# Optimization experiments

Hardware: AMD Instinct MI355X
Metric: run time of the kernel (lower is better)

The kernel has to match this reference:

```python
import jax, jax.numpy as jnp
import numpy as np

PAD = 0
NEG = -1e9
POSV = 1e9

def ln(x, eps=1e-5):
    m = jnp.mean(x, -1, keepdims=True)
    v = jnp.mean((x - m) ** 2, -1, keepdims=True)
    return (x - m) * jax.lax.rsqrt(v + eps)

def conv1d(h, w, b, shift):
    # h: [B,L,H], w: [K,H,H] (WIO). Even kernel -> pad K//2 both sides then drop first output (torch layers.Conv1d shift).
    K = w.shape[0]
    p = K // 2 if shift else (K - 1) // 2
    out = jax.lax.conv_general_dilated(h, w, (1,), [(p, p)], dimension_numbers=('NWC', 'WIO', 'NWC')) + b
    return out[:, 1:, :] if shift else out

def _forward(x, pos, emb, parser_conv_w, parser_conv_b, dist_conv_w, dist_conv_b, dist_lin_w, dist_lin_b, height_w1, height_b1, height_w2, height_b2, rel_weight_raw, scaler_raw, attn_ln_g, attn_ln_b, qw, qb, kw, kb, vw, vb, ow, ob, ff_ln_g, ff_ln_b, ff_w1, ff_b1, ff_w2, ff_b2, final_ln_g, final_ln_b, out_bias):
    B, L = x.shape
    NL, NH, _ = rel_weight_raw.shape
    H = emb.shape[1]
    mask = x != PAD
    mask_shift = jnp.concatenate([mask[:, 1:], jnp.zeros((B, 1), bool)], 1)

    # ---- parser: conv + LN(no affine) + tanh stack ----
    h = emb[x]
    for i in range(parser_conv_w.shape[0]):
        h = jnp.where(mask[:, :, None], h, 0.0)
        h = jnp.tanh(ln(conv1d(h, parser_conv_w[i], parser_conv_b[i], False)))
    height = (jnp.tanh(ln(h @ height_w1 + height_b1)) @ height_w2 + height_b2)[..., 0]
    height = jnp.where(mask, height, NEG)
    distance = (jnp.tanh(ln(conv1d(h, dist_conv_w, dist_conv_b, True))) @ dist_lin_w + dist_lin_b)[..., 0]
    distance = jnp.where(mask_shift, distance, POSV)

    # ---- margin normalization of distance vs running height max ----
    hm = jnp.triu(jnp.broadcast_to(height[:, None, :], (B, L, L))) - jnp.tril(jnp.full((B, L, L), POSV, jnp.float32), -1)
    hm = jnp.triu(jax.lax.cummax(hm, axis=2))
    d_pad = jnp.concatenate([jnp.full((B, 1), POSV, jnp.float32), distance[:, :-1]], 1)
    margin = jnp.triu(jnp.minimum(jax.nn.relu(d_pad[:, :, None] - hm), jax.nn.relu(distance[:, None, :] - hm)))
    mm = jnp.concatenate([mask_shift[:, None, :], jnp.broadcast_to(mask[:, None, :], (B, L - 1, L))], 1)
    distance = distance - jnp.max(jnp.where(mm, margin, 0.0))

    # ---- block decomposition via cummin (flip+cummin) and cumsum ----
    scaler = jnp.exp(scaler_raw)
    gamma = jax.nn.sigmoid(-(distance[:, None, :] - height[:, :, None]) * scaler[0])
    ones = jnp.ones_like(gamma)
    bml = jax.lax.cummin(jnp.tril(gamma, -1) + jnp.triu(ones), axis=2, reverse=True)
    bml = jnp.tril(bml - jnp.concatenate([jnp.zeros((B, L, 1)), bml[:, :, :-1]], 2))
    xr = jnp.triu(gamma) + jnp.tril(ones, -1)
    bmr = jax.lax.cummin(jnp.concatenate([jnp.ones((B, L, 1)), xr[:, :, :-1]], 2), axis=2)
    bmr = jnp.triu(bmr - jnp.concatenate([bmr[:, :, 1:], jnp.zeros((B, L, 1))], 2))
    block_p = bml[:, :, :, None] * bmr[:, :, None, :]  # [B,L,L,L]
    block = jnp.tril(jnp.cumsum(bml, 2)) + jnp.triu(jnp.cumsum(bmr[:, :, ::-1], 2)[:, :, ::-1], 1)

    # ---- head distribution: softmax of height over span i<=k<=j ----
    idx = jnp.arange(L)
    hmask = (idx[:, None, None] <= idx[None, None, :]) & (idx[None, None, :] <= idx[None, :, None])
    head_p = jax.nn.softmax(jnp.where(hmask[None], (height * scaler[1])[:, None, None, :], NEG), axis=-1)  # [B,L,L,L]
    head = jnp.einsum('blij,bijh->blh', block_p, head_p)
    eye = jnp.eye(L, dtype=bool)[None]
    head = jnp.where(eye, 0.0, head)
    child = jnp.swapaxes(head, 1, 2)
    cibling = jnp.where(eye, 0.0, head @ child)
    rel = jnp.stack([head, child], 1)  # relations = ('head','child')
    rel_w = jax.nn.softmax(rel_weight_raw, -1)  # weight_act = 'softmax'
    dep = jnp.einsum('lhr,brij->lbhij', rel_w, rel)  # [NL,B,NH,L,L]

    # ---- transformer: sigmoid(QK^T) * structural mask (eval mode, no dropout) ----
    kpm = jnp.where(mask, 0.0, NEG)[:, None, None, :]
    hd = H // NH
    h = emb[x]
    for i in range(NL):
        z = ln(h) * attn_ln_g[i] + attn_ln_b[i]
        q = ((z @ qw[i] + qb[i]) * (hd ** -0.5)).reshape(B, L, NH, hd)
        k = (z @ kw[i] + kb[i]).reshape(B, L, NH, hd)
        v = (z @ vw[i] + vb[i]).reshape(B, L, NH, hd)
        w = jax.nn.sigmoid(jnp.einsum('blhd,bmhd->bhlm', q, k) + kpm) * dep[i]
        o = jnp.einsum('bhlm,bmhd->blhd', w, v).reshape(B, L, H)
        h = h + (o @ ow[i] + ob[i])
        f = ln(h) * ff_ln_g[i] + ff_ln_b[i]
        h = h + (jax.nn.leaky_relu(f @ ff_w1[i] + ff_b1[i]) @ ff_w2[i] + ff_b2[i])
    raw = ln(h) * final_ln_g + final_ln_b
    return (raw @ emb.T + out_bias).reshape(B * L, -1)  # tied output embedding

def setup_inputs():
    key = jax.random.key(0)
    ks = iter(jax.random.split(key, 64))
    B, L, H, V = 8, 128, 512, 10000
    NL, NH, FF = 8, 8, 2048
    def rn(shape, sc=0.02):
        return jax.random.normal(next(ks), shape, jnp.float32) * sc
    return dict(
        x=jax.random.randint(next(ks), (B, L), 0, V),
        pos=jnp.tile(jnp.arange(L)[None, :], (B, 1)),
        emb=rn((V, H), 0.05),
        parser_conv_w=rn((4, 9, H, H)), parser_conv_b=rn((4, H)),
        dist_conv_w=rn((2, H, H)), dist_conv_b=rn((H,)),
        dist_lin_w=rn((H, 1)), dist_lin_b=rn((1,)),
        height_w1=rn((H, H)), height_b1=rn((H,)),
        height_w2=rn((H, 1)), height_b2=rn((1,)),
        rel_weight_raw=rn((NL, NH, 2), 0.1),
        scaler_raw=rn((2,), 0.1),
        attn_ln_g=jnp.ones((NL, H)), attn_ln_b=jnp.zeros((NL, H)),
        qw=rn((NL, H, H)), qb=rn((NL, H)),
        kw=rn((NL, H, H)), kb=rn((NL, H)),
        vw=rn((NL, H, H)), vb=rn((NL, H)),
        ow=rn((NL, H, H)), ob=rn((NL, H)),
        ff_ln_g=jnp.ones((NL, H)), ff_ln_b=jnp.zeros((NL, H)),
        ff_w1=rn((NL, H, FF)), ff_b1=rn((NL, FF)),
        ff_w2=rn((NL, FF, H)), ff_b2=rn((NL, H)),
        final_ln_g=jnp.ones((H,)), final_ln_b=jnp.zeros((H,)),
        out_bias=jnp.zeros((V,)),
    )

def reference(x, pos, emb, parser_conv_w, parser_conv_b, dist_conv_w, dist_conv_b, dist_lin_w, dist_lin_b, height_w1, height_b1, height_w2, height_b2, rel_weight_raw, scaler_raw, attn_ln_g, attn_ln_b, qw, qb, kw, kb, vw, vb, ow, ob, ff_ln_g, ff_ln_b, ff_w1, ff_b1, ff_w2, ff_b2, final_ln_g, final_ln_b, out_bias):
    return _forward(x, pos, emb, parser_conv_w, parser_conv_b, dist_conv_w, dist_conv_b, dist_lin_w, dist_lin_b, height_w1, height_b1, height_w2, height_b2, rel_weight_raw, scaler_raw, attn_ln_g, attn_ln_b, qw, qb, kw, kb, vw, vb, ow, ob, ff_ln_g, ff_ln_b, ff_w1, ff_b1, ff_w2, ff_b2, final_ln_g, final_ln_b, out_bias)
```

## Files before the change

### kernel.cpp

```cpp
#include <hip/hip_runtime.h>
#include <hip/hip_bf16.h>

typedef __hip_bfloat16 bf16;
typedef __attribute__((ext_vector_type(8))) short short8;
typedef __attribute__((ext_vector_type(4))) float f32x4;

static __device__ __forceinline__ float b2f(bf16 x){ return __bfloat162float(x); }
static __device__ __forceinline__ bf16  f2b(float x){ return __float2bfloat16(x); }
static __device__ __forceinline__ short f2bs(float x){ bf16 h = f2b(x); short s; __builtin_memcpy(&s, &h, 2); return s; }

#define GLOBAL_AS __attribute__((address_space(1)))
#define LDS_AS    __attribute__((address_space(3)))
static __device__ __forceinline__ void gll16(const void* g, short* l){
  __builtin_amdgcn_global_load_lds((const GLOBAL_AS void*)g, (LDS_AS void*)l, 16, 0, 0);
}


constexpr size_t AL2(size_t x){ return (x + 255) & ~(size_t)255; }
constexpr size_t SCAL_OFF  = 0;
constexpr size_t BIASF_OFF = AL2(SCAL_OFF + 256*4);
constexpr size_t MASK_OFF  = AL2(BIASF_OFF + 50176*4);
constexpr size_t HEIGHT_OFF= AL2(MASK_OFF + 1024*4);
constexpr size_t DIST_OFF  = AL2(HEIGHT_OFF + 1024*4);
constexpr size_t E_OFF     = AL2(DIST_OFF + 1024*4);
constexpr size_t P_OFF     = AL2(E_OFF + 1024*4);
constexpr size_t H0_OFF    = AL2(P_OFF + 8*132*4);
constexpr size_t TMPF_OFF  = AL2(H0_OFF + (size_t)1024*512*4);
constexpr size_t HMBF_OFF  = AL2(TMPF_OFF + (size_t)1024*512*4);
constexpr size_t HBF_OFF   = AL2(HMBF_OFF + (size_t)1024*512*2);
constexpr size_t ZBF_OFF   = AL2(HBF_OFF + (size_t)1024*512*2);
constexpr size_t QKV_OFF   = AL2(ZBF_OFF + (size_t)1024*512*2);
constexpr size_t VT_OFF    = AL2(QKV_OFF + (size_t)1024*1536*2);
constexpr size_t WATT_OFF  = AL2(VT_OFF + (size_t)64*64*128*2);
constexpr size_t OBF_OFF   = AL2(WATT_OFF + (size_t)64*128*128*2);
constexpr size_t FF1_OFF   = AL2(OBF_OFF + (size_t)1024*512*2);
constexpr size_t ACOL_OFF  = AL2(FF1_OFF + (size_t)1024*2048*2);
constexpr size_t BML_OFF   = AL2(ACOL_OFF + (size_t)1024*4608*2);
constexpr size_t BMR_OFF   = AL2(BML_OFF + (size_t)8*128*128*4);
constexpr size_t HEADP_OFF = AL2(BMR_OFF + (size_t)8*128*128*4);
constexpr size_t PWT_OFF   = AL2(HEADP_OFF + (size_t)8*128*128*4);
constexpr size_t DWT_OFF   = AL2(PWT_OFF + (size_t)4*4608*512*2);
constexpr size_t HW1T_OFF  = AL2(DWT_OFF + (size_t)1024*512*2);
constexpr size_t QKVT_OFF  = AL2(HW1T_OFF + (size_t)512*512*2);
constexpr size_t OWT_OFF   = AL2(QKVT_OFF + (size_t)8*1536*512*2);
constexpr size_t F1T_OFF   = AL2(OWT_OFF + (size_t)8*512*512*2);
constexpr size_t F2T_OFF   = AL2(F1T_OFF + (size_t)8*2048*512*2);
constexpr size_t WS_NEED   = AL2(F2T_OFF + (size_t)8*512*2048*2);

__global__ __launch_bounds__(256) void prep_k(
    const float* pcb, const float* dcb, const float* hb1,
    const float* qb, const float* kb, const float* vb, const float* ob,
    const float* fb1, const float* fb2, const float* outb,
    const float* relraw, const float* sraw,
    float* biasf, float* scal)
{
  int i = blockIdx.x*256 + threadIdx.x;
  if      (i < 2048)  biasf[i] = pcb[i];
  else if (i < 2560)  biasf[i] = dcb[i-2048];
  else if (i < 3072)  biasf[i] = hb1[i-2560];
  else if (i < 15360){ int j = i-3072; int l = j/1536, n = j%1536;
    biasf[i] = (n<512 ? qb[l*512+n] : n<1024 ? kb[l*512+n-512] : vb[l*512+n-1024]); }
  else if (i < 19456) biasf[i] = ob[i-15360];
  else if (i < 35840) biasf[i] = fb1[i-19456];
  else if (i < 39936) biasf[i] = fb2[i-35840];
  else if (i < 49936) biasf[i] = outb[i-39936];
  else if (i == 49936) scal[0] = expf(sraw[0]);
  else if (i == 49937) scal[1] = expf(sraw[1]);
  else if (i == 49938) scal[2] = 0.f;
  else if (i < 49939 + 128){ int q = i - 49939; int p = q>>1;
    float e0 = expf(relraw[2*p]), e1 = expf(relraw[2*p+1]);
    float r0 = e0/(e0+e1);
    scal[4 + q] = (q&1) ? (1.f - r0) : r0; }
}

struct TP {
  const float *pw, *dw, *hw1, *qw, *kw, *vw, *ow, *f1, *f2;
  bf16 *pwT, *dwT, *hw1T, *qkvT, *owT, *f1T, *f2T;
};
__global__ __launch_bounds__(256) void transpose_all_k(TP tp){
  __shared__ short tl[32*33];
  int blk = blockIdx.x, t = threadIdx.x;
  const float* src; bf16* dst; int R, C, tile;
  if      (blk < 9216){ int l = blk/2304; tile = blk%2304; src = tp.pw + (size_t)l*2359296; dst = tp.pwT + (size_t)l*2359296; R=4608; C=512; }
  else if (blk < 9728){ tile = blk-9216; src = tp.dw;  dst = tp.dwT;  R=1024; C=512; }
  else if (blk < 9984){ tile = blk-9728; src = tp.hw1; dst = tp.hw1T; R=512;  C=512; }
  else if (blk < 12032){ int j=blk-9984;  int l=j>>8; tile=j&255;  src = tp.qw + (size_t)l*262144; dst = tp.qkvT + (size_t)l*786432;           R=512; C=512; }
  else if (blk < 14080){ int j=blk-12032; int l=j>>8; tile=j&255;  src = tp.kw + (size_t)l*262144; dst = tp.qkvT + (size_t)l*786432 + 262144;  R=512; C=512; }
  else if (blk < 16128){ int j=blk-14080; int l=j>>8; tile=j&255;  src = tp.vw + (size_t)l*262144; dst = tp.qkvT + (size_t)l*786432 + 524288;  R=512; C=512; }
  else if (blk < 18176){ int j=blk-16128; int l=j>>8; tile=j&255;  src = tp.ow + (size_t)l*262144; dst = tp.owT + (size_t)l*262144;            R=512; C=512; }
  else if (blk < 26368){ int j=blk-18176; int l=j>>10; tile=j&1023; src = tp.f1 + (size_t)l*1048576; dst = tp.f1T + (size_t)l*1048576;         R=512; C=2048; }
  else                 { int j=blk-26368; int l=j>>10; tile=j&1023; src = tp.f2 + (size_t)l*1048576; dst = tp.f2T + (size_t)l*1048576;         R=2048; C=512; }
  int tc = C >> 5;
  int r0 = (tile/tc)*32, c0 = (tile%tc)*32;
  int tx = t & 31, ty = t >> 5;
  short* d = (short*)dst;
  #pragma unroll
  for (int p=0;p<4;p++){ int r = ty + p*8; tl[r*33+tx] = f2bs(src[(size_t)(r0+r)*C + c0 + tx]); }
  __syncthreads();
  #pragma unroll
  for (int p=0;p<4;p++){ int cc = ty + p*8; d[(size_t)(c0+cc)*R + r0 + tx] = tl[tx*33+cc]; }
}

__global__ __launch_bounds__(256) void embed_k(const int* x, const float* emb, float* h0, bf16* hm, int* mask){
  int m = blockIdx.x, t = threadIdx.x;
  int xi = x[m]; int mk = (xi != 0) ? 1 : 0;
  if (t == 0) mask[m] = mk;
  const float* e = emb + (size_t)xi*512;
  float e0 = e[t], e1 = e[t+256];
  h0[(size_t)m*512+t]     = e0;
  h0[(size_t)m*512+t+256] = e1;
  bf16 z = f2b(0.f);
  hm[(size_t)m*512+t]     = mk ? f2b(e0) : z;
  hm[(size_t)m*512+t+256] = mk ? f2b(e1) : z;
}

__global__ __launch_bounds__(256) void embcast_k(const float* e, bf16* o){
  size_t i = (size_t)blockIdx.x*1024 + threadIdx.x*4;
  float4 v = *(const float4*)(e + i);
  o[i]   = f2b(v.x); o[i+1] = f2b(v.y);
  o[i+2] = f2b(v.z); o[i+3] = f2b(v.w);
}

__global__ __launch_bounds__(64) void im2col9_k(const bf16* hsrc, bf16* acol){
  int m = blockIdx.x, k = blockIdx.y, t = threadIdx.x;
  int tt = m & 127; int st = tt + k - 4;
  int4* dst = (int4*)(acol + (size_t)m*4608 + (size_t)k*512);
  if (st >= 0 && st < 128){ const int4* s = (const int4*)(hsrc + (size_t)(m + k - 4)*512); dst[t] = s[t]; }
  else dst[t] = make_int4(0,0,0,0);
}
__global__ __launch_bounds__(64) void im2col2_k(const bf16* hsrc, bf16* acol){
  int m = blockIdx.x, k = blockIdx.y, t = threadIdx.x;
  int tt = m & 127; int st = tt + k;
  int4* dst = (int4*)(acol + (size_t)m*1024 + (size_t)k*512);
  if (st < 128){ const int4* s = (const int4*)(hsrc + (size_t)(m + k)*512); dst[t] = s[t]; }
  else dst[t] = make_int4(0,0,0,0);
}

__device__ __forceinline__ float blkSum256(float v, float* red){
  #pragma unroll
  for (int o=32;o>0;o>>=1) v += __shfl_down(v, o);
  __syncthreads();
  if ((threadIdx.x & 63) == 0) red[threadIdx.x >> 6] = v;
  __syncthreads();
  return red[0]+red[1]+red[2]+red[3];
}
__global__ __launch_bounds__(256) void ln_tanh_k(const float* X, const float* bias, bf16* outm, bf16* outp, const int* mask){
  __shared__ float red[4];
  int row = blockIdx.x, t = threadIdx.x;
  const float* x = X + (size_t)row*512;
  float a0 = x[t] + bias[t], a1 = x[t+256] + bias[t+256];
  float mean = blkSum256(a0+a1, red)*(1.f/512.f);
  float d0 = a0-mean, d1 = a1-mean;
  float var = blkSum256(d0*d0+d1*d1, red)*(1.f/512.f);
  float inv = rsqrtf(var + 1e-5f);
  float y0 = tanhf(d0*inv), y1 = tanhf(d1*inv);
  int mk = mask[row];
  size_t o = (size_t)row*512 + t;
  outp[o] = f2b(y0); outp[o+256] = f2b(y1);
  outm[o] = mk ? f2b(y0) : f2b(0.f);
  outm[o+256] = mk ? f2b(y1) : f2b(0.f);
}
__global__ __launch_bounds__(256) void ln_affine_k(const float* X, const float* g, const float* bb, bf16* out){
  __shared__ float red[4];
  int row = blockIdx.x, t = threadIdx.x;
  const float* x = X + (size_t)row*512;
  float a0 = x[t], a1 = x[t+256];
  float mean = blkSum256(a0+a1, red)*(1.f/512.f);
  float d0 = a0-mean, d1 = a1-mean;
  float var = blkSum256(d0*d0+d1*d1, red)*(1.f/512.f);
  float inv = rsqrtf(var + 1e-5f);
  size_t o = (size_t)row*512 + t;
  out[o]     = f2b(d0*inv*g[t]     + bb[t]);
  out[o+256] = f2b(d1*inv*g[t+256] + bb[t+256]);
}

__global__ __launch_bounds__(256) void rowdot_k(const bf16* X, const float* w, const float* bsc,
                                                const int* mask, float* out, int mode){
  int wv = threadIdx.x>>6, lane = threadIdx.x&63;
  int m = blockIdx.x*4 + wv;
  const bf16* x = X + (size_t)m*512;
  float s = 0.f;
  #pragma unroll
  for (int i=0;i<8;++i){ int c = i*64 + lane; s += b2f(x[c])*w[c]; }
  #pragma unroll
  for (int o=32;o>0;o>>=1) s += __shfl_down(s,o);
  if (lane==0){
    float v = s + bsc[0];
    if (mode==0) out[m] = (mask[m]!=0) ? v : -1e9f;
    else { int tt = m & 127; bool ms = (tt<127) && (mask[m+1]!=0); out[m] = ms ? v : 1e9f; }
  }
}

__global__ __launch_bounds__(128) void margin_k(const float* height, const float* dist, const int* mask, float* scal){
  int b = blockIdx.x, i = threadIdx.x;
  __shared__ float hg[128], ds[128], red[128];
  hg[i] = height[b*128+i]; ds[i] = dist[b*128+i];
  __syncthreads();
  float dpi = (i==0) ? 1e9f : ds[i-1];
  float hmr = -3.0e38f, best = 0.f;
  for (int j=i; j<128; ++j){
    hmr = fmaxf(hmr, hg[j]);
    float mg = fminf(fmaxf(dpi - hmr, 0.f), fmaxf(ds[j] - hmr, 0.f));
    bool mm = (i==0) ? ((j<127) && (mask[b*128+j+1]!=0)) : (mask[b*128+j]!=0);
    if (mm) best = fmaxf(best, mg);
  }
  red[i] = best; __syncthreads();
  for (int s=64; s>0; s>>=1){ if (i<s) red[i] = fmaxf(red[i], red[i+s]); __syncthreads(); }
  if (i==0) atomicMax((unsigned int*)(scal+2), __float_as_uint(red[0]));
}

__global__ __launch_bounds__(128) void ep_k(const float* height, const float* scal, float* e, float* P){
  int b = blockIdx.x, l = threadIdx.x;
  __shared__ float red[128], sc[128];
  float h = height[b*128+l];
  red[l] = h; __syncthreads();
  for (int s=64;s>0;s>>=1){ if (l<s) red[l] = fmaxf(red[l], red[l+s]); __syncthreads(); }
  float hmax = red[0];
  float ev = expf(scal[1]*(h - hmax));
  e[b*128+l] = ev;
  sc[l] = ev; __syncthreads();
  for (int off=1; off<128; off<<=1){
    float a = (l>=off) ? sc[l-off] : 0.f;
    __syncthreads(); sc[l] += a; __syncthreads();
  }
  P[b*132 + l + 1] = sc[l];
  if (l==0) P[b*132] = 0.f;
}

__global__ __launch_bounds__(128) void gbml_k(const float* height, const float* dist, const float* scal,
                                              float* bml, float* bmr){
  int b = blockIdx.x, l = threadIdx.x;
  __shared__ float dAdj[128], hg[128];
  float dmax = scal[2], s0 = scal[0];
  dAdj[l] = dist[b*128+l] - dmax; hg[l] = height[b*128+l];
  __syncthreads();
  float hl = hg[l];
  float* BML = bml + ((size_t)b*128 + l)*128;
  float* BMR = bmr + ((size_t)b*128 + l)*128;
  for (int j=l+1; j<128; ++j) BML[j] = 0.f;
  float cmn = 1.f;
  for (int j=l-1; j>=0; --j){
    float g = 1.f/(1.f + expf(-(hl - dAdj[j])*s0));
    float cmj = fminf(g, cmn);
    BML[j+1] = cmn - cmj;
    cmn = cmj;
  }
  BML[0] = cmn;
  for (int j=0; j<l; ++j) BMR[j] = 0.f;
  float cmp_ = 1.f;
  for (int j=l+1; j<128; ++j){
    float g = 1.f/(1.f + expf(-(hl - dAdj[j-1])*s0));
    float cmj = fminf(g, cmp_);
    BMR[j-1] = cmp_ - cmj;
    cmp_ = cmj;
  }
  BMR[127] = cmp_;
}

__global__ __launch_bounds__(128) void head_k(const float* bml, const float* bmr, const float* e,
                                              const float* P, float* head){
  int bl = blockIdx.x; int b = bl>>7, l = bl&127; int h = threadIdx.x;
  __shared__ float bmlS[128], bmrS[128], eS[128], PS[129], U[128], Vv[128];
  bmlS[h] = bml[(size_t)bl*128 + h];
  bmrS[h] = bmr[(size_t)bl*128 + h];
  eS[h]   = e[b*128+h];
  PS[h]   = P[b*132+h];
  if (h==0) PS[128] = P[b*132+128];
  __syncthreads();
  float u = 0.f, v = 0.f;
  if (h <= l){
    float bh = bmlS[h];
    if (bh > 0.f){
      float ph = PS[h]; float acc = 0.f;
      for (int j=l; j<128; ++j){
        float br = bmrS[j]; float den = PS[j+1] - ph;
        if (br > 0.f && den > 1e-30f) acc += br/den;
      }
      u = bh*acc;
    }
  } else {
    float br = bmrS[h];
    if (br > 0.f){
      float p1 = PS[h+1]; float acc = 0.f;
      for (int i=0;i<=l;++i){
        float bm = bmlS[i]; float den = p1 - PS[i];
        if (bm > 0.f && den > 1e-30f) acc += bm/den;
      }
      v = br*acc;
    }
  }
  U[h] = u; Vv[h] = v; __syncthreads();
  for (int off=1; off<128; off<<=1){
    float a  = (h>=off)      ? U[h-off]  : 0.f;
    float bs = (h+off<128)   ? Vv[h+off] : 0.f;
    __syncthreads();
    U[h] += a; Vv[h] += bs;
    __syncthreads();
  }
  float a = (h<l) ? U[h] : (h>l) ? Vv[h] : 0.f;
  head[(size_t)bl*128 + h] = eS[h]*a;
}

__global__ __launch_bounds__(256) void vtrans_k(const bf16* qkv, bf16* vt){
  __shared__ short tl[64*130];
  const short* q = (const short*)qkv; short* v = (short*)vt;
  int z = blockIdx.x, t = threadIdx.x; int b = z>>3, h = z&7;
  for (int i=t; i<8192; i+=256){ int l = i>>6, d = i&63;
    tl[d*130 + l] = q[((size_t)(b*128+l))*1536 + 1024 + h*64 + d]; }
  __syncthreads();
  for (int i=t; i<8192; i+=256){ v[(size_t)z*8192 + i] = tl[(i>>7)*130 + (i&127)]; }
}

enum GMode { GM_F32=0, GM_BF16=1, GM_LEAKY=2, GM_ADD=3, GM_SIGDEP=4 };

template<int MODE, int SPLIT>
__global__ __launch_bounds__(256) void gemm_nt(
    const bf16* __restrict__ Ab, int lda, long long sA1, long long sA2,
    const bf16* __restrict__ Bb, int ldb, long long sB1, long long sB2,
    void* __restrict__ Cb, int ldc, long long sC1, long long sC2,
    int M, int N, int K, int kchunk,
    const float* __restrict__ bias,
    const int* __restrict__ maskp, const float* __restrict__ headp,
    const float* __restrict__ scal, int layer)
{
  __shared__ short As[2][4096];
  __shared__ short Bs[2][4096];
  const int t = threadIdx.x;
  int zb = 0, zh = 0, kbeg = 0, kend = K;
  if (SPLIT){ kbeg = blockIdx.z*kchunk; kend = min(K, kbeg + kchunk); }
  else { int z = blockIdx.z; zb = z>>3; zh = z&7; }
  const bf16* A  = Ab + (size_t)zb*sA1 + (size_t)zh*sA2 + (size_t)blockIdx.y*64*lda;
  const bf16* Bp = Bb + (size_t)zb*sB1 + (size_t)zh*sB2;
  const int n0 = blockIdx.x*64;
  const int wv = t>>6, ln = t&63;
  const int wm = wv>>1, wn = wv&1;

  f32x4 acc[2][2];
  #pragma unroll
  for (int mi=0;mi<2;++mi)
    #pragma unroll
    for (int ci=0;ci<2;++ci) acc[mi][ci] = (f32x4){0.f,0.f,0.f,0.f};

  auto stage = [&](int buf, int k0){
    #pragma unroll
    for (int q=0;q<2;++q){
      int r0 = wv*16 + q*8;
      int row = r0 + (ln>>3);
      int gs = (ln&7) ^ (row&7);
      gll16(A + (size_t)row*lda + k0 + gs*8, &As[buf][r0*64]);
      int rb = n0 + row; if (rb >= N) rb = N-1;
      gll16(Bp + (size_t)rb*ldb + k0 + gs*8, &Bs[buf][r0*64]);
    }
  };

  const int nIter = (kend - kbeg) >> 6;
  stage(0, kbeg);
  for (int it=0; it<nIter; ++it){
    const int cur = it & 1;
    __syncthreads();
    if (it+1 < nIter) stage(cur^1, kbeg + (it+1)*64);
    #pragma unroll
    for (int kk=0; kk<64; kk+=32){
      short8 av[2], bv[2];
      #pragma unroll
      for (int mi=0;mi<2;++mi){
        int r = wm*32 + mi*16 + (ln&15);
        int gg = (kk>>3) + (ln>>4);
        av[mi] = *(const short8*)(&As[cur][r*64 + ((gg ^ (r&7))<<3)]);
      }
      #pragma unroll
      for (int ci=0;ci<2;++ci){
        int r = wn*32 + ci*16 + (ln&15);
        int gg = (kk>>3) + (ln>>4);
        bv[ci] = *(const short8*)(&Bs[cur][r*64 + ((gg ^ (r&7))<<3)]);
      }
      #pragma unroll
      for (int mi=0;mi<2;++mi)
        #pragma unroll
        for (int ci=0;ci<2;++ci)
          acc[mi][ci] = __builtin_amdgcn_mfma_f32_16x16x32_bf16(av[mi], bv[ci], acc[mi][ci], 0,0,0);
    }
  }

  const int cin = ln & 15;
  #pragma unroll
  for (int mi=0;mi<2;++mi){
    #pragma unroll
    for (int ci=0;ci<2;++ci){
      int col = n0 + wn*32 + ci*16 + cin;
      if (col >= N) continue;
      #pragma unroll
      for (int r=0;r<4;++r){
        int row = blockIdx.y*64 + wm*32 + mi*16 + ((ln>>4)<<2) + r;
        float v = acc[mi][ci][r];
        size_t coff = (size_t)zb*sC1 + (size_t)zh*sC2 + (size_t)row*ldc + col;
        if (MODE == GM_F32){
          if (SPLIT) atomicAdd(((float*)Cb) + coff, v);
          else { if (bias) v += bias[col]; ((float*)Cb)[coff] = v; }
        } else if (MODE == GM_BF16){
          if (bias) v += bias[col];
          ((bf16*)Cb)[coff] = f2b(v);
        } else if (MODE == GM_LEAKY){
          v += bias[col];
          v = (v > 0.f) ? v : 0.01f*v;
          ((bf16*)Cb)[coff] = f2b(v);
        } else if (MODE == GM_ADD){
          float add = (!SPLIT || blockIdx.z == 0) ? bias[col] : 0.f;
          atomicAdd(((float*)Cb) + coff, v + add);
        } else {
          float outv = 0.f;
          if (maskp[zb*128 + col] != 0){
            float sg = 1.f/(1.f + expf(-v*0.125f));
            float h1 = headp[((size_t)zb*128 + row)*128 + col];
            float h2 = headp[((size_t)zb*128 + col)*128 + row];
            float rw0 = scal[4 + (layer*8 + zh)*2];
            float rw1 = scal[4 + (layer*8 + zh)*2 + 1];
            outv = sg*(rw0*h1 + rw1*h2);
          }
          ((bf16*)Cb)[coff] = f2b(outv);
        }
      }
    }
  }
}

extern "C" void kernel_launch(void* const* d_in, const int* in_sizes, int n_in,
                              void* d_out, int out_size, void* d_ws, size_t ws_size,
                              hipStream_t stream)
{
  if (ws_size < WS_NEED) return;
  const int*   x    = (const int*)d_in[0];
  const float* emb  = (const float*)d_in[2];
  const float* pw   = (const float*)d_in[3];
  const float* pcb  = (const float*)d_in[4];
  const float* dw   = (const float*)d_in[5];
  const float* dcb  = (const float*)d_in[6];
  const float* dlw  = (const float*)d_in[7];
  const float* dlb  = (const float*)d_in[8];
  const float* hw1  = (const float*)d_in[9];
  const float* hb1  = (const float*)d_in[10];
  const float* hw2  = (const float*)d_in[11];
  const float* hb2  = (const float*)d_in[12];
  const float* relw = (const float*)d_in[13];
  const float* sraw = (const float*)d_in[14];
  const float* alg  = (const float*)d_in[15];
  const float* alb  = (const float*)d_in[16];
  const float* qw   = (const float*)d_in[17];
  const float* qb   = (const float*)d_in[18];
  const float* kw   = (const float*)d_in[19];
  const float* kb   = (const float*)d_in[20];
  const float* vw   = (const float*)d_in[21];
  const float* vb   = (const float*)d_in[22];
  const float* ow   = (const float*)d_in[23];
  const float* ob   = (const float*)d_in[24];
  const float* flg  = (const float*)d_in[25];
  const float* flb  = (const float*)d_in[26];
  const float* f1   = (const float*)d_in[27];
  const float* fb1  = (const float*)d_in[28];
  const float* f2   = (const float*)d_in[29];
  const float* fb2  = (const float*)d_in[30];
  const float* fng  = (const float*)d_in[31];
  const float* fnb  = (const float*)d_in[32];
  const float* outb = (const float*)d_in[33];

  char* ws = (char*)d_ws;
  float* scal    = (float*)(ws + SCAL_OFF);
  float* biasf   = (float*)(ws + BIASF_OFF);
  int*   maskp   = (int*)(ws + MASK_OFF);
  float* heightp = (float*)(ws + HEIGHT_OFF);
  float* distp   = (float*)(ws + DIST_OFF);
  float* e_p     = (float*)(ws + E_OFF);
  float* P_p     = (float*)(ws + P_OFF);
  float* h0      = (float*)(ws + H0_OFF);
  float* tmpf    = (float*)(ws + TMPF_OFF);
  bf16* hm_bf    = (bf16*)(ws + HMBF_OFF);
  bf16* h_bf     = (bf16*)(ws + HBF_OFF);
  bf16* z_bf     = (bf16*)(ws + ZBF_OFF);
  bf16* qkvp     = (bf16*)(ws + QKV_OFF);
  bf16* vtp      = (bf16*)(ws + VT_OFF);
  bf16* wattp    = (bf16*)(ws + WATT_OFF);
  bf16* o_bf     = (bf16*)(ws + OBF_OFF);
  bf16* ff1p     = (bf16*)(ws + FF1_OFF);
  bf16* acol     = (bf16*)(ws + ACOL_OFF);
  float* bmlp    = (float*)(ws + BML_OFF);
  float* bmrp    = (float*)(ws + BMR_OFF);
  float* headp   = (float*)(ws + HEADP_OFF);
  bf16* pwT      = (bf16*)(ws + PWT_OFF);
  bf16* dwT      = (bf16*)(ws + DWT_OFF);
  bf16* hw1T     = (bf16*)(ws + HW1T_OFF);
  bf16* qkvT     = (bf16*)(ws + QKVT_OFF);
  bf16* owT      = (bf16*)(ws + OWT_OFF);
  bf16* f1T      = (bf16*)(ws + F1T_OFF);
  bf16* f2T      = (bf16*)(ws + F2T_OFF);
  bf16* embB     = (bf16*)(ws + QKV_OFF);

  prep_k<<<196,256,0,stream>>>(pcb,dcb,hb1,qb,kb,vb,ob,fb1,fb2,outb,relw,sraw,biasf,scal);
  TP tp{pw,dw,hw1,qw,kw,vw,ow,f1,f2, pwT,dwT,hw1T,qkvT,owT,f1T,f2T};
  transpose_all_k<<<34560,256,0,stream>>>(tp);
  embed_k<<<1024,256,0,stream>>>(x, emb, h0, hm_bf, maskp);

  const size_t TMPB = (size_t)1024*512*4;
  for (int i=0;i<4;++i){
    im2col9_k<<<dim3(1024,9),64,0,stream>>>(hm_bf, acol);
    hipMemsetAsync(tmpf, 0, TMPB, stream);
    gemm_nt<GM_F32,1><<<dim3(8,16,6),256,0,stream>>>(acol,4608,0,0, pwT+(size_t)i*2359296,4608,0,0,
        tmpf,512,0,0, 1024,512,4608,768, nullptr, nullptr,nullptr,nullptr,0);
    ln_tanh_k<<<1024,256,0,stream>>>(tmpf, biasf + i*512, hm_bf, h_bf, maskp);
  }
  hipMemsetAsync(tmpf, 0, TMPB, stream);
  gemm_nt<GM_F32,1><<<dim3(8,16,2),256,0,stream>>>(h_bf,512,0,0, hw1T,512,0,0,
      tmpf,512,0,0, 1024,512,512,256, nullptr, nullptr,nullptr,nullptr,0);
  ln_tanh_k<<<1024,256,0,stream>>>(tmpf, biasf + 2560, hm_bf, z_bf, maskp);
  rowdot_k<<<256,256,0,stream>>>(z_bf, hw2, hb2, maskp, heightp, 0);
  ep_k<<<8,128,0,stream>>>(heightp, scal, e_p, P_p);
  im2col2_k<<<dim3(1024,2),64,0,stream>>>(h_bf, acol);
  hipMemsetAsync(tmpf, 0, TMPB, stream);
  gemm_nt<GM_F32,1><<<dim3(8,16,2),256,0,stream>>>(acol,1024,0,0, dwT,1024,0,0,
      tmpf,512,0,0, 1024,512,1024,512, nullptr, nullptr,nullptr,nullptr,0);
  ln_tanh_k<<<1024,256,0,stream>>>(tmpf, biasf + 2048, hm_bf, z_bf, maskp);
  rowdot_k<<<256,256,0,stream>>>(z_bf, dlw, dlb, maskp, distp, 1);
  margin_k<<<8,128,0,stream>>>(heightp, distp, maskp, scal);
  gbml_k<<<8,128,0,stream>>>(heightp, distp, scal, bmlp, bmrp);
  head_k<<<1024,128,0,stream>>>(bmlp, bmrp, e_p, P_p, headp);

  for (int l=0;l<8;++l){
    ln_affine_k<<<1024,256,0,stream>>>(h0, alg + l*512, alb + l*512, z_bf);
    gemm_nt<GM_BF16,0><<<dim3(24,16,1),256,0,stream>>>(z_bf,512,0,0, qkvT+(size_t)l*786432,512,0,0,
        qkvp,1536,0,0, 1024,1536,512,0, biasf + 3072 + l*1536, nullptr,nullptr,nullptr,0);
    vtrans_k<<<64,256,0,stream>>>(qkvp, vtp);
    gemm_nt<GM_SIGDEP,0><<<dim3(2,2,64),256,0,stream>>>(qkvp,1536,196608,64, qkvp+512,1536,196608,64,
        wattp,128,131072,16384, 128,128,64,0, nullptr, maskp, headp, scal, l);
    gemm_nt<GM_BF16,0><<<dim3(1,2,64),256,0,stream>>>(wattp,128,131072,16384, vtp,128,65536,8192,
        o_bf,512,65536,64, 128,64,128,0, nullptr, nullptr,nullptr,nullptr,0);
    gemm_nt<GM_ADD,1><<<dim3(8,16,2),256,0,stream>>>(o_bf,512,0,0, owT+(size_t)l*262144,512,0,0,
        h0,512,0,0, 1024,512,512,256, biasf + 15360 + l*512, nullptr,nullptr,nullptr,0);
    ln_affine_k<<<1024,256,0,stream>>>(h0, flg + l*512, flb + l*512, z_bf);
    gemm_nt<GM_LEAKY,0><<<dim3(32,16,1),256,0,stream>>>(z_bf,512,0,0, f1T+(size_t)l*1048576,512,0,0,
        ff1p,2048,0,0, 1024,2048,512,0, biasf + 19456 + l*2048, nullptr,nullptr,nullptr,0);
    gemm_nt<GM_ADD,1><<<dim3(8,16,4),256,0,stream>>>(ff1p,2048,0,0, f2T+(size_t)l*1048576,2048,0,0,
        h0,512,0,0, 1024,512,2048,512, biasf + 35840 + l*512, nullptr,nullptr,nullptr,0);
  }
  ln_affine_k<<<1024,256,0,stream>>>(h0, fng, fnb, z_bf);
  embcast_k<<<5000,256,0,stream>>>(emb, embB);
  gemm_nt<GM_F32,0><<<dim3(157,16,1),256,0,stream>>>(z_bf,512,0,0, embB,512,0,0,
      d_out,10000,0,0, 1024,10000,512,0, biasf + 39936, nullptr,nullptr,nullptr,0);
}
```

Baseline: 1.085 ms.

## Template GEMM tile sizes, widen transpose tiles, merge im2col launches

The GEMM kernel gains template parameters for tile M/N and single or double buffering. Larger 128x128 or 64x128 tiles are used for the conv, FFN, QKV and output-projection GEMMs to get more operand reuse per block. The weight transpose now uses 64x64 tiles with float4 loads and 16-byte bf16 stores, and the im2col kernels are reworked into one launch dimension with more threads per block. Larger tiles cut the block count, which may hurt occupancy on small GEMMs, and single buffering gives up load/compute overlap.

```diff
diff --git a/kernel.cpp b/kernel.cpp
--- a/kernel.cpp
+++ b/kernel.cpp
@@ -78,27 +78,38 @@
   bf16 *pwT, *dwT, *hw1T, *qkvT, *owT, *f1T, *f2T;
 };
 __global__ __launch_bounds__(256) void transpose_all_k(TP tp){
-  __shared__ short tl[32*33];
+  __shared__ float tl[64*69];
   int blk = blockIdx.x, t = threadIdx.x;
   const float* src; bf16* dst; int R, C, tile;
-  if      (blk < 9216){ int l = blk/2304; tile = blk%2304; src = tp.pw + (size_t)l*2359296; dst = tp.pwT + (size_t)l*2359296; R=4608; C=512; }
-  else if (blk < 9728){ tile = blk-9216; src = tp.dw;  dst = tp.dwT;  R=1024; C=512; }
-  else if (blk < 9984){ tile = blk-9728; src = tp.hw1; dst = tp.hw1T; R=512;  C=512; }
-  else if (blk < 12032){ int j=blk-9984;  int l=j>>8; tile=j&255;  src = tp.qw + (size_t)l*262144; dst = tp.qkvT + (size_t)l*786432;           R=512; C=512; }
-  else if (blk < 14080){ int j=blk-12032; int l=j>>8; tile=j&255;  src = tp.kw + (size_t)l*262144; dst = tp.qkvT + (size_t)l*786432 + 262144;  R=512; C=512; }
-  else if (blk < 16128){ int j=blk-14080; int l=j>>8; tile=j&255;  src = tp.vw + (size_t)l*262144; dst = tp.qkvT + (size_t)l*786432 + 524288;  R=512; C=512; }
-  else if (blk < 18176){ int j=blk-16128; int l=j>>8; tile=j&255;  src = tp.ow + (size_t)l*262144; dst = tp.owT + (size_t)l*262144;            R=512; C=512; }
-  else if (blk < 26368){ int j=blk-18176; int l=j>>10; tile=j&1023; src = tp.f1 + (size_t)l*1048576; dst = tp.f1T + (size_t)l*1048576;         R=512; C=2048; }
-  else                 { int j=blk-26368; int l=j>>10; tile=j&1023; src = tp.f2 + (size_t)l*1048576; dst = tp.f2T + (size_t)l*1048576;         R=2048; C=512; }
-  int tc = C >> 5;
-  int r0 = (tile/tc)*32, c0 = (tile%tc)*32;
-  int tx = t & 31, ty = t >> 5;
+  if      (blk < 2304){ int l = blk/576; tile = blk%576; src = tp.pw + (size_t)l*2359296; dst = tp.pwT + (size_t)l*2359296; R=4608; C=512; }
+  else if (blk < 2432){ tile = blk-2304; src = tp.dw;  dst = tp.dwT;  R=1024; C=512; }
+  else if (blk < 2496){ tile = blk-2432; src = tp.hw1; dst = tp.hw1T; R=512;  C=512; }
+  else if (blk < 3008){ int j=blk-2496;  int l=j>>6; tile=j&63;  src = tp.qw + (size_t)l*262144; dst = tp.qkvT + (size_t)l*786432;           R=512; C=512; }
+  else if (blk < 3520){ int j=blk-3008;  int l=j>>6; tile=j&63;  src = tp.kw + (size_t)l*262144; dst = tp.qkvT + (size_t)l*786432 + 262144;  R=512; C=512; }
+  else if (blk < 4032){ int j=blk-3520;  int l=j>>6; tile=j&63;  src = tp.vw + (size_t)l*262144; dst = tp.qkvT + (size_t)l*786432 + 524288;  R=512; C=512; }
+  else if (blk < 4544){ int j=blk-4032;  int l=j>>6; tile=j&63;  src = tp.ow + (size_t)l*262144; dst = tp.owT + (size_t)l*262144;            R=512; C=512; }
+  else if (blk < 6592){ int j=blk-4544;  int l=j>>8; tile=j&255; src = tp.f1 + (size_t)l*1048576; dst = tp.f1T + (size_t)l*1048576;         R=512; C=2048; }
+  else                { int j=blk-6592;  int l=j>>8; tile=j&255; src = tp.f2 + (size_t)l*1048576; dst = tp.f2T + (size_t)l*1048576;         R=2048; C=512; }
+  int tc = C >> 6;
+  int r0 = (tile/tc)*64, c0 = (tile%tc)*64;
+  #pragma unroll
+  for (int p=0;p<4;p++){
+    int r = p*16 + (t>>4);
+    float4 v = *(const float4*)(src + (size_t)(r0+r)*C + c0 + (t&15)*4);
+    float* row = &tl[r*69 + (t&15)*4];
+    row[0]=v.x; row[1]=v.y; row[2]=v.z; row[3]=v.w;
+  }
+  __syncthreads();
   short* d = (short*)dst;
   #pragma unroll
-  for (int p=0;p<4;p++){ int r = ty + p*8; tl[r*33+tx] = f2bs(src[(size_t)(r0+r)*C + c0 + tx]); }
-  __syncthreads();
-  #pragma unroll
-  for (int p=0;p<4;p++){ int cc = ty + p*8; d[(size_t)(c0+cc)*R + r0 + tx] = tl[tx*33+cc]; }
+  for (int p=0;p<2;p++){
+    int c = p*32 + (t>>3);
+    int rr = (t&7)*8;
+    short s[8];
+    #pragma unroll
+    for (int j=0;j<8;j++) s[j] = f2bs(tl[(rr+j)*69 + c]);
+    *(int4*)(d + (size_t)(c0+c)*R + r0 + rr) = *(int4*)s;
+  }
 }
 
 __global__ __launch_bounds__(256) void embed_k(const int* x, const float* emb, float* h0, bf16* hm, int* mask){
@@ -121,19 +132,26 @@
   o[i+2] = f2b(v.z); o[i+3] = f2b(v.w);
 }
 
-__global__ __launch_bounds__(64) void im2col9_k(const bf16* hsrc, bf16* acol){
-  int m = blockIdx.x, k = blockIdx.y, t = threadIdx.x;
-  int tt = m & 127; int st = tt + k - 4;
-  int4* dst = (int4*)(acol + (size_t)m*4608 + (size_t)k*512);
-  if (st >= 0 && st < 128){ const int4* s = (const int4*)(hsrc + (size_t)(m + k - 4)*512); dst[t] = s[t]; }
-  else dst[t] = make_int4(0,0,0,0);
-}
-__global__ __launch_bounds__(64) void im2col2_k(const bf16* hsrc, bf16* acol){
-  int m = blockIdx.x, k = blockIdx.y, t = threadIdx.x;
-  int tt = m & 127; int st = tt + k;
-  int4* dst = (int4*)(acol + (size_t)m*1024 + (size_t)k*512);
-  if (st < 128){ const int4* s = (const int4*)(hsrc + (size_t)(m + k)*512); dst[t] = s[t]; }
-  else dst[t] = make_int4(0,0,0,0);
+__global__ __launch_bounds__(256) void im2col9_k(const bf16* hsrc, bf16* acol){
+  int m = blockIdx.x, t = threadIdx.x;
+  int tt = m & 127;
+  int4* dst = (int4*)(acol + (size_t)m*4608);
+  for (int j=t; j<576; j+=256){
+    int k = j>>6, e = j&63;
+    int st = tt + k - 4;
+    int4 v = make_int4(0,0,0,0);
+    if (st>=0 && st<128) v = ((const int4*)(hsrc + (size_t)(m+k-4)*512))[e];
+    dst[j] = v;
+  }
+}
+__global__ __launch_bounds__(128) void im2col2_k(const bf16* hsrc, bf16* acol){
+  int m = blockIdx.x, t = threadIdx.x;
+  int tt = m & 127;
+  int k = t>>6, e = t&63;
+  int st = tt + k;
+  int4 v = make_int4(0,0,0,0);
+  if (st < 128) v = ((const int4*)(hsrc + (size_t)(m+k)*512))[e];
+  ((int4*)(acol + (size_t)m*1024))[t] = v;
 }
 
 __device__ __forceinline__ float blkSum256(float v, float* red){
@@ -313,7 +331,7 @@
 
 enum GMode { GM_F32=0, GM_BF16=1, GM_LEAKY=2, GM_ADD=3, GM_SIGDEP=4 };
 
-template<int MODE, int SPLIT>
+template<int MODE, int SPLIT, int TM, int TN, int DB>
 __global__ __launch_bounds__(256) void gemm_nt(
     const bf16* __restrict__ Ab, int lda, long long sA1, long long sA2,
     const bf16* __restrict__ Bb, int ldb, long long sB1, long long sB2,
@@ -323,75 +341,94 @@
     const int* __restrict__ maskp, const float* __restrict__ headp,
     const float* __restrict__ scal, int layer)
 {
-  __shared__ short As[2][4096];
-  __shared__ short Bs[2][4096];
+  constexpr int FM = TM/32, FN = TN/32;
+  __shared__ short As[DB][TM*64];
+  __shared__ short Bs[DB][TN*64];
   const int t = threadIdx.x;
   int zb = 0, zh = 0, kbeg = 0, kend = K;
   if (SPLIT){ kbeg = blockIdx.z*kchunk; kend = min(K, kbeg + kchunk); }
   else { int z = blockIdx.z; zb = z>>3; zh = z&7; }
-  const bf16* A  = Ab + (size_t)zb*sA1 + (size_t)zh*sA2 + (size_t)blockIdx.y*64*lda;
+  const bf16* A  = Ab + (size_t)zb*sA1 + (size_t)zh*sA2 + (size_t)blockIdx.y*TM*lda;
   const bf16* Bp = Bb + (size_t)zb*sB1 + (size_t)zh*sB2;
-  const int n0 = blockIdx.x*64;
+  const int n0 = blockIdx.x*TN;
   const int wv = t>>6, ln = t&63;
   const int wm = wv>>1, wn = wv&1;
 
-  f32x4 acc[2][2];
-  #pragma unroll
-  for (int mi=0;mi<2;++mi)
+  f32x4 acc[FM][FN];
+  #pragma unroll
+  for (int mi=0;mi<FM;++mi)
     #pragma unroll
-    for (int ci=0;ci<2;++ci) acc[mi][ci] = (f32x4){0.f,0.f,0.f,0.f};
+    for (int ci=0;ci<FN;++ci) acc[mi][ci] = (f32x4){0.f,0.f,0.f,0.f};
 
   auto stage = [&](int buf, int k0){
     #pragma unroll
-    for (int q=0;q<2;++q){
-      int r0 = wv*16 + q*8;
+    for (int q=0;q<TM/32;++q){
+      int r0 = wv*(TM/4) + q*8;
       int row = r0 + (ln>>3);
       int gs = (ln&7) ^ (row&7);
       gll16(A + (size_t)row*lda + k0 + gs*8, &As[buf][r0*64]);
+    }
+    #pragma unroll
+    for (int q=0;q<TN/32;++q){
+      int r0 = wv*(TN/4) + q*8;
+      int row = r0 + (ln>>3);
+      int gs = (ln&7) ^ (row&7);
       int rb = n0 + row; if (rb >= N) rb = N-1;
       gll16(Bp + (size_t)rb*ldb + k0 + gs*8, &Bs[buf][r0*64]);
     }
   };
-
-  const int nIter = (kend - kbeg) >> 6;
-  stage(0, kbeg);
-  for (int it=0; it<nIter; ++it){
-    const int cur = it & 1;
-    __syncthreads();
-    if (it+1 < nIter) stage(cur^1, kbeg + (it+1)*64);
+  auto compute = [&](int buf){
     #pragma unroll
     for (int kk=0; kk<64; kk+=32){
-      short8 av[2], bv[2];
+      short8 av[FM], bv[FN];
       #pragma unroll
-      for (int mi=0;mi<2;++mi){
-        int r = wm*32 + mi*16 + (ln&15);
+      for (int mi=0;mi<FM;++mi){
+        int r = wm*(TM/2) + mi*16 + (ln&15);
         int gg = (kk>>3) + (ln>>4);
-        av[mi] = *(const short8*)(&As[cur][r*64 + ((gg ^ (r&7))<<3)]);
+        av[mi] = *(const short8*)(&As[buf][r*64 + ((gg ^ (r&7))<<3)]);
       }
       #pragma unroll
-      for (int ci=0;ci<2;++ci){
-        int r = wn*32 + ci*16 + (ln&15);
+      for (int ci=0;ci<FN;++ci){
+        int r = wn*(TN/2) + ci*16 + (ln&15);
         int gg = (kk>>3) + (ln>>4);
-        bv[ci] = *(const short8*)(&Bs[cur][r*64 + ((gg ^ (r&7))<<3)]);
+        bv[ci] = *(const short8*)(&Bs[buf][r*64 + ((gg ^ (r&7))<<3)]);
       }
       #pragma unroll
-      for (int mi=0;mi<2;++mi)
+      for (int mi=0;mi<FM;++mi)
         #pragma unroll
-        for (int ci=0;ci<2;++ci)
+        for (int ci=0;ci<FN;++ci)
           acc[mi][ci] = __builtin_amdgcn_mfma_f32_16x16x32_bf16(av[mi], bv[ci], acc[mi][ci], 0,0,0);
     }
+  };
+
+  const int nIter = (kend - kbeg) >> 6;
+  if (DB == 2){
+    stage(0, kbeg);
+    for (int it=0; it<nIter; ++it){
+      const int cur = it & 1;
+      __syncthreads();
+      if (it+1 < nIter) stage(cur^1, kbeg + (it+1)*64);
+      compute(cur);
+    }
+  } else {
+    for (int it=0; it<nIter; ++it){
+      if (it) __syncthreads();
+      stage(0, kbeg + it*64);
+      __syncthreads();
+      compute(0);
+    }
   }
 
   const int cin = ln & 15;
   #pragma unroll
-  for (int mi=0;mi<2;++mi){
+  for (int mi=0;mi<FM;++mi){
     #pragma unroll
-    for (int ci=0;ci<2;++ci){
-      int col = n0 + wn*32 + ci*16 + cin;
+    for (int ci=0;ci<FN;++ci){
+      int col = n0 + wn*(TN/2) + ci*16 + cin;
       if (col >= N) continue;
       #pragma unroll
       for (int r=0;r<4;++r){
-        int row = blockIdx.y*64 + wm*32 + mi*16 + ((ln>>4)<<2) + r;
+        int row = blockIdx.y*TM + wm*(TM/2) + mi*16 + ((ln>>4)<<2) + r;
         float v = acc[mi][ci][r];
         size_t coff = (size_t)zb*sC1 + (size_t)zh*sC2 + (size_t)row*ldc + col;
         if (MODE == GM_F32){
@@ -496,26 +533,26 @@
 
   prep_k<<<196,256,0,stream>>>(pcb,dcb,hb1,qb,kb,vb,ob,fb1,fb2,outb,relw,sraw,biasf,scal);
   TP tp{pw,dw,hw1,qw,kw,vw,ow,f1,f2, pwT,dwT,hw1T,qkvT,owT,f1T,f2T};
-  transpose_all_k<<<34560,256,0,stream>>>(tp);
+  transpose_all_k<<<8640,256,0,stream>>>(tp);
   embed_k<<<1024,256,0,stream>>>(x, emb, h0, hm_bf, maskp);
 
   const size_t TMPB = (size_t)1024*512*4;
   for (int i=0;i<4;++i){
-    im2col9_k<<<dim3(1024,9),64,0,stream>>>(hm_bf, acol);
+    im2col9_k<<<1024,256,0,stream>>>(hm_bf, acol);
     hipMemsetAsync(tmpf, 0, TMPB, stream);
-    gemm_nt<GM_F32,1><<<dim3(8,16,6),256,0,stream>>>(acol,4608,0,0, pwT+(size_t)i*2359296,4608,0,0,
+    gemm_nt<GM_F32,1,128,128,1><<<dim3(4,8,6),256,0,stream>>>(acol,4608,0,0, pwT+(size_t)i*2359296,4608,0,0,
         tmpf,512,0,0, 1024,512,4608,768, nullptr, nullptr,nullptr,nullptr,0);
     ln_tanh_k<<<1024,256,0,stream>>>(tmpf, biasf + i*512, hm_bf, h_bf, maskp);
   }
   hipMemsetAsync(tmpf, 0, TMPB, stream);
-  gemm_nt<GM_F32,1><<<dim3(8,16,2),256,0,stream>>>(h_bf,512,0,0, hw1T,512,0,0,
+  gemm_nt<GM_F32,1,64,64,2><<<dim3(8,16,2),256,0,stream>>>(h_bf,512,0,0, hw1T,512,0,0,
       tmpf,512,0,0, 1024,512,512,256, nullptr, nullptr,nullptr,nullptr,0);
   ln_tanh_k<<<1024,256,0,stream>>>(tmpf, biasf + 2560, hm_bf, z_bf, maskp);
   rowdot_k<<<256,256,0,stream>>>(z_bf, hw2, hb2, maskp, heightp, 0);
   ep_k<<<8,128,0,stream>>>(heightp, scal, e_p, P_p);
-  im2col2_k<<<dim3(1024,2),64,0,stream>>>(h_bf, acol);
+  im2col2_k<<<1024,128,0,stream>>>(h_bf, acol);
   hipMemsetAsync(tmpf, 0, TMPB, stream);
-  gemm_nt<GM_F32,1><<<dim3(8,16,2),256,0,stream>>>(acol,1024,0,0, dwT,1024,0,0,
+  gemm_nt<GM_F32,1,64,64,2><<<dim3(8,16,2),256,0,stream>>>(acol,1024,0,0, dwT,1024,0,0,
       tmpf,512,0,0, 1024,512,1024,512, nullptr, nullptr,nullptr,nullptr,0);
   ln_tanh_k<<<1024,256,0,stream>>>(tmpf, biasf + 2048, hm_bf, z_bf, maskp);
   rowdot_k<<<256,256,0,stream>>>(z_bf, dlw, dlb, maskp, distp, 1);
@@ -525,23 +562,23 @@
 
   for (int l=0;l<8;++l){
     ln_affine_k<<<1024,256,0,stream>>>(h0, alg + l*512, alb + l*512, z_bf);
-    gemm_nt<GM_BF16,0><<<dim3(24,16,1),256,0,stream>>>(z_bf,512,0,0, qkvT+(size_t)l*786432,512,0,0,
+    gemm_nt<GM_BF16,0,64,128,1><<<dim3(12,16,1),256,0,stream>>>(z_bf,512,0,0, qkvT+(size_t)l*786432,512,0,0,
         qkvp,1536,0,0, 1024,1536,512,0, biasf + 3072 + l*1536, nullptr,nullptr,nullptr,0);
     vtrans_k<<<64,256,0,stream>>>(qkvp, vtp);
-    gemm_nt<GM_SIGDEP,0><<<dim3(2,2,64),256,0,stream>>>(qkvp,1536,196608,64, qkvp+512,1536,196608,64,
+    gemm_nt<GM_SIGDEP,0,64,64,2><<<dim3(2,2,64),256,0,stream>>>(qkvp,1536,196608,64, qkvp+512,1536,196608,64,
         wattp,128,131072,16384, 128,128,64,0, nullptr, maskp, headp, scal, l);
-    gemm_nt<GM_BF16,0><<<dim3(1,2,64),256,0,stream>>>(wattp,128,131072,16384, vtp,128,65536,8192,
+    gemm_nt<GM_BF16,0,64,64,2><<<dim3(1,2,64),256,0,stream>>>(wattp,128,131072,16384, vtp,128,65536,8192,
         o_bf,512,65536,64, 128,64,128,0, nullptr, nullptr,nullptr,nullptr,0);
-    gemm_nt<GM_ADD,1><<<dim3(8,16,2),256,0,stream>>>(o_bf,512,0,0, owT+(size_t)l*262144,512,0,0,
+    gemm_nt<GM_ADD,1,64,64,2><<<dim3(8,16,2),256,0,stream>>>(o_bf,512,0,0, owT+(size_t)l*262144,512,0,0,
         h0,512,0,0, 1024,512,512,256, biasf + 15360 + l*512, nullptr,nullptr,nullptr,0);
     ln_affine_k<<<1024,256,0,stream>>>(h0, flg + l*512, flb + l*512, z_bf);
-    gemm_nt<GM_LEAKY,0><<<dim3(32,16,1),256,0,stream>>>(z_bf,512,0,0, f1T+(size_t)l*1048576,512,0,0,
+    gemm_nt<GM_LEAKY,0,64,128,1><<<dim3(16,16,1),256,0,stream>>>(z_bf,512,0,0, f1T+(size_t)l*1048576,512,0,0,
         ff1p,2048,0,0, 1024,2048,512,0, biasf + 19456 + l*2048, nullptr,nullptr,nullptr,0);
-    gemm_nt<GM_ADD,1><<<dim3(8,16,4),256,0,stream>>>(ff1p,2048,0,0, f2T+(size_t)l*1048576,2048,0,0,
+    gemm_nt<GM_ADD,1,64,128,1><<<dim3(4,16,4),256,0,stream>>>(ff1p,2048,0,0, f2T+(size_t)l*1048576,2048,0,0,
         h0,512,0,0, 1024,512,2048,512, biasf + 35840 + l*512, nullptr,nullptr,nullptr,0);
   }
   ln_affine_k<<<1024,256,0,stream>>>(h0, fng, fnb, z_bf);
   embcast_k<<<5000,256,0,stream>>>(emb, embB);
-  gemm_nt<GM_F32,0><<<dim3(157,16,1),256,0,stream>>>(z_bf,512,0,0, embB,512,0,0,
+  gemm_nt<GM_F32,0,128,128,1><<<dim3(79,8,1),256,0,stream>>>(z_bf,512,0,0, embB,512,0,0,
       d_out,10000,0,0, 1024,10000,512,0, biasf + 39936, nullptr,nullptr,nullptr,0);
 }
```

Result: slower. 1.194 ms (+10.0%).
